# Kernel optimization log

Hardware: AMD Instinct MI355X
Metric: run time of the kernel (lower is better)

The kernel has to match this reference:

```python
import jax, jax.numpy as jnp
import numpy as np

NUM_HEADS = 16
THETA = 10000.0

def _rope(t, token_ids, theta):
    # t: [B, H, S, Dk]; token_ids: [S]
    d_k = t.shape[-1]
    inv_freq = theta ** (-jnp.arange(0, d_k, 2, dtype=jnp.float32) / d_k)  # [Dk/2]
    ang = token_ids.astype(jnp.float32)[:, None] * inv_freq[None, :]       # [S, Dk/2]
    cos, sin = jnp.cos(ang), jnp.sin(ang)
    x1, x2 = t[..., ::2], t[..., 1::2]
    r1 = x1 * cos - x2 * sin
    r2 = x1 * sin + x2 * cos
    return jnp.stack([r1, r2], axis=-1).reshape(t.shape)

def setup_inputs() -> dict:
    key = jax.random.key(0)
    ks = jax.random.split(key, 5)
    d_model = 1024
    scale = 0.02
    return {
        "x": jax.random.normal(ks[0], (4, 2048, d_model), dtype=jnp.float32),
        "token_ids": jnp.arange(2048, dtype=jnp.int32),
        "Wq": jax.random.normal(ks[1], (d_model, d_model), dtype=jnp.float32) * scale,
        "Wk": jax.random.normal(ks[2], (d_model, d_model), dtype=jnp.float32) * scale,
        "Wv": jax.random.normal(ks[3], (d_model, d_model), dtype=jnp.float32) * scale,
        "Wo": jax.random.normal(ks[4], (d_model, d_model), dtype=jnp.float32) * scale,
    }

def reference(x, token_ids, Wq, Wk, Wv, Wo):
    B, S, D = x.shape
    H = NUM_HEADS
    Dk = D // H
    def split_heads(t):
        return t.reshape(B, S, H, Dk).transpose(0, 2, 1, 3)  # [B,H,S,Dk]
    q = split_heads(x @ Wq.T)
    k = split_heads(x @ Wk.T)
    v = split_heads(x @ Wv.T)
    q = _rope(q, token_ids, THETA)
    k = _rope(k, token_ids, THETA)
    scores = jnp.einsum("bhqd,bhkd->bhqk", q, k) / jnp.sqrt(jnp.float32(Dk))
    causal = jnp.tril(jnp.ones((S, S), dtype=bool))
    scores = jnp.where(causal, scores, jnp.float32(-1e9))
    attn = jax.nn.softmax(scores, axis=-1)
    out = jnp.einsum("bhqk,bhkd->bhqd", attn, v)
    out = out.transpose(0, 2, 1, 3).reshape(B, S, H * Dk)
    return out @ Wo.T
```

## Files before the change

kernel.cpp:

```cpp
#include <hip/hip_runtime.h>

#define BATCH 4
#define SLEN 2048
#define DMODEL 1024
#define NHEADS 16
#define DK 64
#define MROWS (BATCH * SLEN)
#define NQB 16
#define SCALE_LOG2E 0.1803368801111731f

typedef short bf16x8 __attribute__((ext_vector_type(8)));
typedef unsigned short u16x4 __attribute__((ext_vector_type(4)));
typedef float f32x4 __attribute__((ext_vector_type(4)));

__device__ __forceinline__ unsigned short f2bf(float f) {
    unsigned u = __float_as_uint(f);
    unsigned r = u + 0x7FFFu + ((u >> 16) & 1u);
    return (unsigned short)(r >> 16);
}

__device__ __forceinline__ unsigned pkbf(float a, float b) {
    unsigned r;
    asm volatile("v_cvt_pk_bf16_f32 %0, %1, %2" : "=v"(r) : "v"(a), "v"(b));
    return r;
}

__device__ __forceinline__ void gload_lds16(const void* g, void* l) {
    __builtin_amdgcn_global_load_lds(
        (const __attribute__((address_space(1))) void*)g,
        (__attribute__((address_space(3))) void*)l, 16, 0, 0);
}

__global__ void cvt_f32_bf16(const float* __restrict__ in, unsigned short* __restrict__ out, int n) {
    int i = (blockIdx.x * blockDim.x + threadIdx.x) * 4;
    if (i >= n) return;
    float4 v = *reinterpret_cast<const float4*>(in + i);
    u16x4 o;
    o[0] = f2bf(v.x); o[1] = f2bf(v.y); o[2] = f2bf(v.z); o[3] = f2bf(v.w);
    *reinterpret_cast<u16x4*>(out + i) = o;
}

__global__ void cvt_w_all(const float* __restrict__ w0, const float* __restrict__ w1,
                          const float* __restrict__ w2, const float* __restrict__ w3,
                          unsigned short* __restrict__ o0, unsigned short* __restrict__ o1,
                          unsigned short* __restrict__ o2, unsigned short* __restrict__ o3) {
    int z = blockIdx.y;
    const float* src = (z == 0) ? w0 : (z == 1) ? w1 : (z == 2) ? w2 : w3;
    unsigned short* dst = (z == 0) ? o0 : (z == 1) ? o1 : (z == 2) ? o2 : o3;
    int i = (blockIdx.x * blockDim.x + threadIdx.x) * 4;
    float4 v = *reinterpret_cast<const float4*>(src + i);
    u16x4 o;
    o[0] = f2bf(v.x); o[1] = f2bf(v.y); o[2] = f2bf(v.z); o[3] = f2bf(v.w);
    *reinterpret_cast<u16x4*>(dst + i) = o;
}

__global__ void rope_table(const int* __restrict__ tok, float* __restrict__ cs, float* __restrict__ sn) {
    int idx = blockIdx.x * blockDim.x + threadIdx.x;
    if (idx >= SLEN * 32) return;
    int s = idx >> 5, fi = idx & 31;
    float invf = powf(10000.0f, -(float)(2 * fi) / 64.0f);
    float ang = (float)tok[s] * invf;
    cs[idx] = cosf(ang);
    sn[idx] = sinf(ang);
}

__global__ __launch_bounds__(256) void qkv_gemm(
    const unsigned short* __restrict__ X,
    const unsigned short* __restrict__ Wq,
    const unsigned short* __restrict__ Wk,
    const unsigned short* __restrict__ Wv,
    const float* __restrict__ cs_tab, const float* __restrict__ sn_tab,
    unsigned short* __restrict__ Q, unsigned short* __restrict__ K,
    unsigned short* __restrict__ VT)
{
    __shared__ alignas(16) unsigned short Bs[3][64 * 64];
    const int tid = threadIdx.x, lane = tid & 63, wave = tid >> 6;
    const int ln = lane & 15, kq = lane >> 4;
    const int wr = wave >> 1, wc = wave & 1;
    const int m0 = blockIdx.x * 128;
    const int n0 = blockIdx.y * 64;
    const unsigned short* Ws[3] = {Wq, Wk, Wv};

    f32x4 acc[3][4][2];
#pragma unroll
    for (int z = 0; z < 3; z++)
#pragma unroll
        for (int a = 0; a < 4; a++)
#pragma unroll
            for (int b = 0; b < 2; b++) acc[z][a][b] = (f32x4){0.f, 0.f, 0.f, 0.f};

    const unsigned short* Abase = X + (size_t)(m0 + wr * 64 + ln) * DMODEL + kq * 8;

    for (int k0 = 0; k0 < DMODEL; k0 += 64) {
        if (k0) __syncthreads();
#pragma unroll
        for (int z = 0; z < 3; z++)
#pragma unroll
            for (int i = 0; i < 2; i++) {
                int s = i * 256 + tid;
                int r = s >> 3;
                int u = (s & 7) ^ (r & 7);
                gload_lds16(Ws[z] + (size_t)(n0 + r) * DMODEL + k0 + u * 8,
                            &Bs[z][(i * 256 + wave * 64) * 8]);
            }
        __syncthreads();

        bf16x8 af[4][2];
#pragma unroll
        for (int mt = 0; mt < 4; mt++)
#pragma unroll
            for (int kc = 0; kc < 2; kc++)
                af[mt][kc] = *reinterpret_cast<const bf16x8*>(
                    Abase + (size_t)mt * 16 * DMODEL + k0 + kc * 32);

#pragma unroll
        for (int z = 0; z < 3; z++) {
            bf16x8 bfr[2][2];
#pragma unroll
            for (int nt = 0; nt < 2; nt++) {
                int row = wc * 32 + nt * 16 + ln;
#pragma unroll
                for (int kc = 0; kc < 2; kc++) {
                    int u = (kc * 4 + kq) ^ (row & 7);
                    bfr[nt][kc] = *reinterpret_cast<const bf16x8*>(&Bs[z][row * 64 + u * 8]);
                }
            }
            __builtin_amdgcn_s_setprio(1);
#pragma unroll
            for (int kc = 0; kc < 2; kc++)
#pragma unroll
                for (int mt = 0; mt < 4; mt++)
#pragma unroll
                    for (int nt = 0; nt < 2; nt++)
                        acc[z][mt][nt] = __builtin_amdgcn_mfma_f32_16x16x32_bf16(
                            af[mt][kc], bfr[nt][kc], acc[z][mt][nt], 0, 0, 0);
            __builtin_amdgcn_s_setprio(0);
        }
    }

    int m0w = m0 + wr * 64;
    int n0w = n0 + wc * 32;
#pragma unroll
    for (int z = 0; z < 2; z++) {
        unsigned short* dst = z ? K : Q;
#pragma unroll
        for (int nt = 0; nt < 2; nt++) {
            int n = n0w + nt * 16 + ln;
            int h = n >> 6, d = n & 63;
            int fi = d >> 1;
#pragma unroll
            for (int mt = 0; mt < 4; mt++) {
#pragma unroll
                for (int j = 0; j < 4; j++) {
                    int m = m0w + mt * 16 + kq * 4 + j;
                    int b = m >> 11, s = m & (SLEN - 1);
                    float v = acc[z][mt][nt][j];
                    float c = cs_tab[s * 32 + fi];
                    float si = sn_tab[s * 32 + fi];
                    float p = __shfl_xor(v, 1);
                    v = (d & 1) ? (p * si + v * c) : (v * c - p * si);
                    if (z == 0) v *= SCALE_LOG2E;
                    dst[(((size_t)(b * NHEADS + h) * SLEN + s) << 6) + d] = f2bf(v);
                }
            }
        }
    }
#pragma unroll
    for (int nt = 0; nt < 2; nt++) {
        int n = n0w + nt * 16 + ln;
        int h = n >> 6, d = n & 63;
#pragma unroll
        for (int mt = 0; mt < 4; mt++) {
#pragma unroll
            for (int j = 0; j < 4; j++) {
                int m = m0w + mt * 16 + kq * 4 + j;
                int b = m >> 11, s = m & (SLEN - 1);
                VT[((size_t)(b * NHEADS + h) * DK + d) * SLEN + s] = f2bf(acc[2][mt][nt][j]);
            }
        }
    }
}

__device__ __forceinline__ void gemm128_core_sb(
    const unsigned short* __restrict__ A, const unsigned short* __restrict__ B,
    int m0, int n0, int tid, f32x4 (&acc)[4][4],
    unsigned short* As, unsigned short* Bs)
{
    int lane = tid & 63, wave = tid >> 6;
    int ln = lane & 15, kq = lane >> 4;
    int wr = wave >> 1, wc = wave & 1;
#pragma unroll
    for (int a = 0; a < 4; a++)
#pragma unroll
        for (int b = 0; b < 4; b++) acc[a][b] = (f32x4){0.f, 0.f, 0.f, 0.f};

    for (int k0 = 0; k0 < DMODEL; k0 += 64) {
        if (k0) __syncthreads();
#pragma unroll
        for (int i = 0; i < 4; i++) {
            int s = i * 256 + tid;
            int r = s >> 3;
            int u = (s & 7) ^ (r & 7);
            gload_lds16(A + (size_t)(m0 + r) * DMODEL + k0 + u * 8, &As[(i * 256 + wave * 64) * 8]);
            gload_lds16(B + (size_t)(n0 + r) * DMODEL + k0 + u * 8, &Bs[(i * 256 + wave * 64) * 8]);
        }
        __syncthreads();

        bf16x8 af[4][2], bfr[4][2];
#pragma unroll
        for (int mt = 0; mt < 4; mt++) {
            int row = wr * 64 + mt * 16 + ln;
#pragma unroll
            for (int kc = 0; kc < 2; kc++) {
                int u = (kc * 4 + kq) ^ (row & 7);
                af[mt][kc] = *reinterpret_cast<const bf16x8*>(&As[row * 64 + u * 8]);
            }
        }
#pragma unroll
        for (int nt = 0; nt < 4; nt++) {
            int row = wc * 64 + nt * 16 + ln;
#pragma unroll
            for (int kc = 0; kc < 2; kc++) {
                int u = (kc * 4 + kq) ^ (row & 7);
                bfr[nt][kc] = *reinterpret_cast<const bf16x8*>(&Bs[row * 64 + u * 8]);
            }
        }
        __builtin_amdgcn_s_setprio(1);
#pragma unroll
        for (int kc = 0; kc < 2; kc++)
#pragma unroll
            for (int mt = 0; mt < 4; mt++)
#pragma unroll
                for (int nt = 0; nt < 4; nt++)
                    acc[mt][nt] = __builtin_amdgcn_mfma_f32_16x16x32_bf16(af[mt][kc], bfr[nt][kc], acc[mt][nt], 0, 0, 0);
        __builtin_amdgcn_s_setprio(0);
    }
}

__global__ __launch_bounds__(512, 4) void attn_kernel(
    const unsigned short* __restrict__ Q, const unsigned short* __restrict__ K,
    const unsigned short* __restrict__ VT, unsigned short* __restrict__ O)
{
    __shared__ alignas(16) unsigned short Kt[2][4096];
    __shared__ alignas(16) unsigned short Vt[2][4096];

    int tid = threadIdx.x, lane = tid & 63, wave = tid >> 6;
    int ln = lane & 15, kq = lane >> 4;
    int qb = blockIdx.x;
    int h = blockIdx.y, b = blockIdx.z;
    size_t headoff = ((size_t)b * NHEADS + h) * SLEN * DK;
    const unsigned short* Qh = Q + headoff;
    const unsigned short* Kh = K + headoff;
    const unsigned short* Vh = VT + headoff;

    auto stage = [&](int buf, int t) {
        int kv0 = t << 6;
        int s = tid;
        int r = s >> 3;
        int cb = (s & 7) ^ (r & 7);
        int rp = ((r >> 5) << 5) | (((r >> 2) & 3) << 3) | (((r >> 4) & 1) << 2) | (r & 3);
        gload_lds16(Kh + (size_t)(kv0 + rp) * DK + cb * 8, &Kt[buf][(wave * 64) * 8]);
        gload_lds16(Vh + (size_t)r * SLEN + kv0 + cb * 8, &Vt[buf][(wave * 64) * 8]);
    };

    const int q0A = (NQB - 1 - qb) * 128 + wave * 16;
    const int q0B = qb * 128 + wave * 16;
    const int ntA = 2 * (NQB - 1 - qb) + 2;
    const int tmaxA = (q0A + 15) >> 6;
    const int tmaxB = (q0B + 15) >> 6;

    bf16x8 aqA[2], aqB[2];
#pragma unroll
    for (int kc = 0; kc < 2; kc++) {
        aqA[kc] = *reinterpret_cast<const bf16x8*>(Qh + (size_t)(q0A + ln) * DK + kc * 32 + kq * 8);
        aqB[kc] = *reinterpret_cast<const bf16x8*>(Qh + (size_t)(q0B + ln) * DK + kc * 32 + kq * 8);
    }

    f32x4 oaccA[4], oaccB[4];
#pragma unroll
    for (int nt = 0; nt < 4; nt++) {
        oaccA[nt] = (f32x4){0.f, 0.f, 0.f, 0.f};
        oaccB[nt] = (f32x4){0.f, 0.f, 0.f, 0.f};
    }
    float mA = -1e30f, lA = 0.f, mB = -1e30f, lB = 0.f;

    stage(0, 0);
    __syncthreads();

    for (int t = 0; t < ntA; t++) {
        int buf = t & 1;
        if (t + 1 < ntA) stage(buf ^ 1, t + 1);
        int kv0 = t << 6;

        auto strip = [&](int q0, bf16x8 (&aq)[2], f32x4 (&oacc)[4], float& m_r, float& l_r) {
            f32x4 sacc[4];
#pragma unroll
            for (int nt = 0; nt < 4; nt++) sacc[nt] = (f32x4){0.f, 0.f, 0.f, 0.f};
            __builtin_amdgcn_s_setprio(1);
#pragma unroll
            for (int nt = 0; nt < 4; nt++) {
                int rr = nt * 16 + ln;
#pragma unroll
                for (int kc = 0; kc < 2; kc++) {
                    int unit = (kc * 4 + kq) ^ (rr & 7);
                    bf16x8 bk = *reinterpret_cast<const bf16x8*>(&Kt[buf][rr * 64 + unit * 8]);
                    sacc[nt] = __builtin_amdgcn_mfma_f32_16x16x32_bf16(bk, aq[kc], sacc[nt], 0, 0, 0);
                }
            }
            __builtin_amdgcn_s_setprio(0);

            if (kv0 + 63 > q0) {
                int q = q0 + ln;
#pragma unroll
                for (int nt = 0; nt < 4; nt++)
#pragma unroll
                    for (int j = 0; j < 4; j++) {
                        int k = kv0 + (nt >> 1) * 32 + kq * 8 + (nt & 1) * 4 + j;
                        if (k > q) sacc[nt][j] = -1e30f;
                    }
            }

            f32x4 m4 = sacc[0];
#pragma unroll
            for (int nt = 1; nt < 4; nt++) {
                m4[0] = fmaxf(m4[0], sacc[nt][0]);
                m4[1] = fmaxf(m4[1], sacc[nt][1]);
                m4[2] = fmaxf(m4[2], sacc[nt][2]);
                m4[3] = fmaxf(m4[3], sacc[nt][3]);
            }
            float mloc = fmaxf(fmaxf(m4[0], m4[1]), fmaxf(m4[2], m4[3]));
            mloc = fmaxf(mloc, __shfl_xor(mloc, 16));
            mloc = fmaxf(mloc, __shfl_xor(mloc, 32));

            bool needscale = !__all(mloc <= m_r + 8.0f);
            float so = 1.f;
            if (needscale) {
                float mn = fmaxf(m_r, mloc);
                so = exp2f(m_r - mn);
                m_r = mn;
            }

            float rs = 0.f;
#pragma unroll
            for (int nt = 0; nt < 4; nt++)
#pragma unroll
                for (int j = 0; j < 4; j++) {
                    float p = exp2f(sacc[nt][j] - m_r);
                    sacc[nt][j] = p;
                    rs += p;
                }
            rs += __shfl_xor(rs, 16);
            rs += __shfl_xor(rs, 32);
            l_r = l_r * so + rs;

            if (needscale) {
                float so_o[4];
#pragma unroll
                for (int j = 0; j < 4; j++) so_o[j] = __shfl(so, kq * 4 + j, 16);
#pragma unroll
                for (int nt = 0; nt < 4; nt++)
#pragma unroll
                    for (int j = 0; j < 4; j++)
                        oacc[nt][j] *= so_o[j];
            }

            bf16x8 pa[2];
#pragma unroll
            for (int kc = 0; kc < 2; kc++) {
                union { unsigned u[4]; bf16x8 v; } r;
                r.u[0] = pkbf(sacc[2 * kc][0], sacc[2 * kc][1]);
                r.u[1] = pkbf(sacc[2 * kc][2], sacc[2 * kc][3]);
                r.u[2] = pkbf(sacc[2 * kc + 1][0], sacc[2 * kc + 1][1]);
                r.u[3] = pkbf(sacc[2 * kc + 1][2], sacc[2 * kc + 1][3]);
                pa[kc] = r.v;
            }

            __builtin_amdgcn_s_setprio(1);
#pragma unroll
            for (int nt = 0; nt < 4; nt++) {
                int rr = nt * 16 + ln;
#pragma unroll
                for (int kc = 0; kc < 2; kc++) {
                    int unit = (kc * 4 + kq) ^ (rr & 7);
                    bf16x8 bv = *reinterpret_cast<const bf16x8*>(&Vt[buf][rr * 64 + unit * 8]);
                    oacc[nt] = __builtin_amdgcn_mfma_f32_16x16x32_bf16(pa[kc], bv, oacc[nt], 0, 0, 0);
                }
            }
            __builtin_amdgcn_s_setprio(0);
        };

        if (t <= tmaxA) strip(q0A, aqA, oaccA, mA, lA);
        if (t <= tmaxB) strip(q0B, aqB, oaccB, mB, lB);

        __syncthreads();
    }

    {
        float lo[4];
#pragma unroll
        for (int j = 0; j < 4; j++) lo[j] = __shfl(lA, kq * 4 + j, 16);
#pragma unroll
        for (int nt = 0; nt < 4; nt++)
#pragma unroll
            for (int j = 0; j < 4; j++) {
                int row = q0A + kq * 4 + j;
                O[((size_t)b * SLEN + row) * DMODEL + h * 64 + nt * 16 + ln] = f2bf(oaccA[nt][j] / lo[j]);
            }
    }
    {
        float lo[4];
#pragma unroll
        for (int j = 0; j < 4; j++) lo[j] = __shfl(lB, kq * 4 + j, 16);
#pragma unroll
        for (int nt = 0; nt < 4; nt++)
#pragma unroll
            for (int j = 0; j < 4; j++) {
                int row = q0B + kq * 4 + j;
                O[((size_t)b * SLEN + row) * DMODEL + h * 64 + nt * 16 + ln] = f2bf(oaccB[nt][j] / lo[j]);
            }
    }
}

__global__ __launch_bounds__(256) void out_gemm(
    const unsigned short* __restrict__ A, const unsigned short* __restrict__ Wo,
    float* __restrict__ out)
{
    __shared__ alignas(16) unsigned short As[128 * 64];
    __shared__ alignas(16) unsigned short Bs[128 * 64];
    int tid = threadIdx.x, lane = tid & 63, wave = tid >> 6;
    int ln = lane & 15, kq = lane >> 4;
    int wr = wave >> 1, wc = wave & 1;
    int m0 = blockIdx.x * 128;
    int n0 = blockIdx.y * 128;

    f32x4 acc[4][4];
    gemm128_core_sb(A, Wo, m0, n0, tid, acc, As, Bs);

    int m0w = m0 + wr * 64, n0w = n0 + wc * 64;
#pragma unroll
    for (int mt = 0; mt < 4; mt++)
#pragma unroll
        for (int nt = 0; nt < 4; nt++)
#pragma unroll
            for (int j = 0; j < 4; j++) {
                int m = m0w + mt * 16 + kq * 4 + j;
                int n = n0w + nt * 16 + ln;
                out[(size_t)m * DMODEL + n] = acc[mt][nt][j];
            }
}

extern "C" void kernel_launch(void* const* d_in, const int* in_sizes, int n_in,
                              void* d_out, int out_size, void* d_ws, size_t ws_size,
                              hipStream_t stream) {
    const float* x  = (const float*)d_in[0];
    const int* tok  = (const int*)d_in[1];
    const float* wq = (const float*)d_in[2];
    const float* wk = (const float*)d_in[3];
    const float* wv = (const float*)d_in[4];
    const float* wo = (const float*)d_in[5];
    float* out = (float*)d_out;

    const size_t XB_OFF = 0;
    const size_t WQ_OFF = 16777216;
    const size_t WK_OFF = 18874368;
    const size_t WV_OFF = 20971520;
    const size_t WO_OFF = 23068672;
    const size_t Q_OFF  = 25165824;
    const size_t K_OFF  = 41943040;
    const size_t VT_OFF = 58720256;
    const size_t O_OFF  = 75497472;
    const size_t CS_OFF = 92274688;
    const size_t SN_OFF = 92536832;
    const size_t WS_NEEDED = 92798976;
    if (ws_size < WS_NEEDED) return;

    char* ws = (char*)d_ws;
    unsigned short* Xb  = (unsigned short*)(ws + XB_OFF);
    unsigned short* Wqb = (unsigned short*)(ws + WQ_OFF);
    unsigned short* Wkb = (unsigned short*)(ws + WK_OFF);
    unsigned short* Wvb = (unsigned short*)(ws + WV_OFF);
    unsigned short* Wob = (unsigned short*)(ws + WO_OFF);
    unsigned short* Qb  = (unsigned short*)(ws + Q_OFF);
    unsigned short* Kb  = (unsigned short*)(ws + K_OFF);
    unsigned short* VTb = (unsigned short*)(ws + VT_OFF);
    unsigned short* Ob  = (unsigned short*)(ws + O_OFF);
    float* cs_tab = (float*)(ws + CS_OFF);
    float* sn_tab = (float*)(ws + SN_OFF);

    cvt_f32_bf16<<<8192, 256, 0, stream>>>(x, Xb, MROWS * DMODEL);
    cvt_w_all<<<dim3(1024, 4), 256, 0, stream>>>(wq, wk, wv, wo, Wqb, Wkb, Wvb, Wob);
    rope_table<<<256, 256, 0, stream>>>(tok, cs_tab, sn_tab);

    qkv_gemm<<<dim3(MROWS / 128, DMODEL / 64, 1), 256, 0, stream>>>(
        Xb, Wqb, Wkb, Wvb, cs_tab, sn_tab, Qb, Kb, VTb);

    attn_kernel<<<dim3(SLEN / 256, NHEADS, BATCH), 512, 0, stream>>>(Qb, Kb, VTb, Ob);

    out_gemm<<<dim3(MROWS / 128, DMODEL / 128, 1), 256, 0, stream>>>(Ob, Wob, out);
}
```

Before: 260.2 us.

## Restructure QKV GEMM into 256x256 LDS-tiled, double-buffered pipelined kernel

The QKV projection now uses 512-thread blocks that each compute a 256x256 output tile for a single weight matrix, selected by blockIdx.y. Previously each block computed 128x64 tiles for all three weights and read X straight from global memory. Both X and W tiles are now staged in swizzled LDS using async global-to-LDS loads, split into halves and double-buffered across k-steps with explicit vmcnt waits and barriers. This raises operand reuse per byte loaded and overlaps loads with MFMA work. In exchange it uses about 128KB of LDS per block, adds more barriers, and launches only 384 blocks, which may leave the last wave underfilled.

```diff
diff --git a/kernel.cpp b/kernel.cpp
--- a/kernel.cpp
+++ b/kernel.cpp
@@ -64,7 +64,7 @@
     sn[idx] = sinf(ang);
 }
 
-__global__ __launch_bounds__(256) void qkv_gemm(
+__global__ __launch_bounds__(512, 2) void qkv_gemm(
     const unsigned short* __restrict__ X,
     const unsigned short* __restrict__ Wq,
     const unsigned short* __restrict__ Wk,
@@ -73,110 +73,137 @@
     unsigned short* __restrict__ Q, unsigned short* __restrict__ K,
     unsigned short* __restrict__ VT)
 {
-    __shared__ alignas(16) unsigned short Bs[3][64 * 64];
+    __shared__ alignas(16) unsigned short Al[2][2][128 * 64];
+    __shared__ alignas(16) unsigned short Bl[2][2][128 * 64];
     const int tid = threadIdx.x, lane = tid & 63, wave = tid >> 6;
     const int ln = lane & 15, kq = lane >> 4;
-    const int wr = wave >> 1, wc = wave & 1;
-    const int m0 = blockIdx.x * 128;
-    const int n0 = blockIdx.y * 64;
-    const unsigned short* Ws[3] = {Wq, Wk, Wv};
-
-    f32x4 acc[3][4][2];
-#pragma unroll
-    for (int z = 0; z < 3; z++)
-#pragma unroll
-        for (int a = 0; a < 4; a++)
-#pragma unroll
-            for (int b = 0; b < 2; b++) acc[z][a][b] = (f32x4){0.f, 0.f, 0.f, 0.f};
-
-    const unsigned short* Abase = X + (size_t)(m0 + wr * 64 + ln) * DMODEL + kq * 8;
-
-    for (int k0 = 0; k0 < DMODEL; k0 += 64) {
-        if (k0) __syncthreads();
-#pragma unroll
-        for (int z = 0; z < 3; z++)
-#pragma unroll
-            for (int i = 0; i < 2; i++) {
-                int s = i * 256 + tid;
-                int r = s >> 3;
-                int u = (s & 7) ^ (r & 7);
-                gload_lds16(Ws[z] + (size_t)(n0 + r) * DMODEL + k0 + u * 8,
-                            &Bs[z][(i * 256 + wave * 64) * 8]);
-            }
-        __syncthreads();
-
-        bf16x8 af[4][2];
-#pragma unroll
-        for (int mt = 0; mt < 4; mt++)
+    const int wm = wave >> 2, wn = wave & 3;
+    const int m0 = blockIdx.x * 256;
+    const int z = blockIdx.y >> 2;
+    const int n0 = (blockIdx.y & 3) * 256;
+    const unsigned short* W = (z == 0) ? Wq : (z == 1) ? Wk : Wv;
+
+    auto stA = [&](int buf, int mh, int kt) {
+#pragma unroll
+        for (int l = 0; l < 2; l++) {
+            int s = l * 512 + tid;
+            int pr = s >> 3;
+            int u = (s & 7) ^ (pr & 7);
+            int grow = m0 + ((pr >> 6) << 7) + mh * 64 + (pr & 63);
+            gload_lds16(X + (size_t)grow * DMODEL + kt * 64 + u * 8,
+                        &Al[buf][mh][(l * 512 + wave * 64) * 8]);
+        }
+    };
+    auto stB = [&](int buf, int nh, int kt) {
+#pragma unroll
+        for (int l = 0; l < 2; l++) {
+            int s = l * 512 + tid;
+            int pc = s >> 3;
+            int u = (s & 7) ^ (pc & 7);
+            int gcol = n0 + ((pc >> 5) << 6) + nh * 32 + (pc & 31);
+            gload_lds16(W + (size_t)gcol * DMODEL + kt * 64 + u * 8,
+                        &Bl[buf][nh][(l * 512 + wave * 64) * 8]);
+        }
+    };
+
+    f32x4 acc[8][4];
+#pragma unroll
+    for (int a = 0; a < 8; a++)
+#pragma unroll
+        for (int b = 0; b < 4; b++) acc[a][b] = (f32x4){0.f, 0.f, 0.f, 0.f};
+
+    stA(0, 0, 0); stB(0, 0, 0); stA(0, 1, 0); stB(0, 1, 0);
+    stA(1, 0, 1); stB(1, 0, 1);
+    asm volatile("s_waitcnt vmcnt(0)" ::: "memory");
+    __builtin_amdgcn_s_barrier();
+
+    const int NK = DMODEL / 64;
+    for (int kt = 0; kt < NK; ++kt) {
+        const int buf = kt & 1;
+#pragma unroll
+        for (int p = 0; p < 4; ++p) {
+            const int mh = p >> 1, nh = p & 1;
+            bf16x8 af[4][2], bq[2][2];
+#pragma unroll
+            for (int i = 0; i < 4; i++) {
+                int pr = wm * 64 + i * 16 + ln;
+#pragma unroll
+                for (int kc = 0; kc < 2; kc++) {
+                    int u = (kc * 4 + kq) ^ (pr & 7);
+                    af[i][kc] = *reinterpret_cast<const bf16x8*>(&Al[buf][mh][(pr * 8 + u) * 8]);
+                }
+            }
+#pragma unroll
+            for (int f = 0; f < 2; f++) {
+                int pc = wn * 32 + f * 16 + ln;
+#pragma unroll
+                for (int kc = 0; kc < 2; kc++) {
+                    int u = (kc * 4 + kq) ^ (pc & 7);
+                    bq[f][kc] = *reinterpret_cast<const bf16x8*>(&Bl[buf][nh][(pc * 8 + u) * 8]);
+                }
+            }
+            if (p == 0 && kt + 1 < NK) stA(buf ^ 1, 1, kt + 1);
+            if (p == 1 && kt + 1 < NK) stB(buf ^ 1, 1, kt + 1);
+            if (p == 2 && kt + 2 < NK) stA(buf, 0, kt + 2);
+            if (p == 3 && kt + 2 < NK) stB(buf, 0, kt + 2);
+            if (kt == NK - 1) {
+                if (p == 0) { asm volatile("s_waitcnt vmcnt(0)" ::: "memory"); }
+            } else {
+                asm volatile("s_waitcnt vmcnt(6)" ::: "memory");
+            }
+            __builtin_amdgcn_s_barrier();
+            asm volatile("s_waitcnt lgkmcnt(0)" ::: "memory");
+            __builtin_amdgcn_sched_barrier(0);
+            __builtin_amdgcn_s_setprio(1);
 #pragma unroll
             for (int kc = 0; kc < 2; kc++)
-                af[mt][kc] = *reinterpret_cast<const bf16x8*>(
-                    Abase + (size_t)mt * 16 * DMODEL + k0 + kc * 32);
-
-#pragma unroll
-        for (int z = 0; z < 3; z++) {
-            bf16x8 bfr[2][2];
-#pragma unroll
-            for (int nt = 0; nt < 2; nt++) {
-                int row = wc * 32 + nt * 16 + ln;
-#pragma unroll
-                for (int kc = 0; kc < 2; kc++) {
-                    int u = (kc * 4 + kq) ^ (row & 7);
-                    bfr[nt][kc] = *reinterpret_cast<const bf16x8*>(&Bs[z][row * 64 + u * 8]);
-                }
-            }
-            __builtin_amdgcn_s_setprio(1);
-#pragma unroll
-            for (int kc = 0; kc < 2; kc++)
-#pragma unroll
-                for (int mt = 0; mt < 4; mt++)
-#pragma unroll
-                    for (int nt = 0; nt < 2; nt++)
-                        acc[z][mt][nt] = __builtin_amdgcn_mfma_f32_16x16x32_bf16(
-                            af[mt][kc], bfr[nt][kc], acc[z][mt][nt], 0, 0, 0);
+#pragma unroll
+                for (int i = 0; i < 4; i++)
+#pragma unroll
+                    for (int f = 0; f < 2; f++)
+                        acc[mh * 4 + i][nh * 2 + f] = __builtin_amdgcn_mfma_f32_16x16x32_bf16(
+                            af[i][kc], bq[f][kc], acc[mh * 4 + i][nh * 2 + f], 0, 0, 0);
             __builtin_amdgcn_s_setprio(0);
-        }
-    }
-
-    int m0w = m0 + wr * 64;
-    int n0w = n0 + wc * 32;
-#pragma unroll
-    for (int z = 0; z < 2; z++) {
+            __builtin_amdgcn_s_barrier();
+        }
+    }
+
+    if (z < 2) {
         unsigned short* dst = z ? K : Q;
 #pragma unroll
-        for (int nt = 0; nt < 2; nt++) {
-            int n = n0w + nt * 16 + ln;
+        for (int b = 0; b < 4; b++) {
+            int n = n0 + wn * 64 + (b >> 1) * 32 + (b & 1) * 16 + ln;
             int h = n >> 6, d = n & 63;
             int fi = d >> 1;
 #pragma unroll
-            for (int mt = 0; mt < 4; mt++) {
+            for (int a = 0; a < 8; a++) {
 #pragma unroll
                 for (int j = 0; j < 4; j++) {
-                    int m = m0w + mt * 16 + kq * 4 + j;
-                    int b = m >> 11, s = m & (SLEN - 1);
-                    float v = acc[z][mt][nt][j];
+                    int m = m0 + wm * 128 + (a >> 2) * 64 + (a & 3) * 16 + kq * 4 + j;
+                    int bb = m >> 11, s = m & (SLEN - 1);
+                    float v = acc[a][b][j];
                     float c = cs_tab[s * 32 + fi];
                     float si = sn_tab[s * 32 + fi];
-                    float p = __shfl_xor(v, 1);
-                    v = (d & 1) ? (p * si + v * c) : (v * c - p * si);
+                    float pz = __shfl_xor(v, 1);
+                    v = (d & 1) ? (pz * si + v * c) : (v * c - pz * si);
                     if (z == 0) v *= SCALE_LOG2E;
-                    dst[(((size_t)(b * NHEADS + h) * SLEN + s) << 6) + d] = f2bf(v);
-                }
-            }
-        }
-    }
-#pragma unroll
-    for (int nt = 0; nt < 2; nt++) {
-        int n = n0w + nt * 16 + ln;
-        int h = n >> 6, d = n & 63;
-#pragma unroll
-        for (int mt = 0; mt < 4; mt++) {
-#pragma unroll
-            for (int j = 0; j < 4; j++) {
-                int m = m0w + mt * 16 + kq * 4 + j;
-                int b = m >> 11, s = m & (SLEN - 1);
-                VT[((size_t)(b * NHEADS + h) * DK + d) * SLEN + s] = f2bf(acc[2][mt][nt][j]);
-            }
+                    dst[(((size_t)(bb * NHEADS + h) * SLEN + s) << 6) + d] = f2bf(v);
+                }
+            }
+        }
+    } else {
+#pragma unroll
+        for (int b = 0; b < 4; b++) {
+            int n = n0 + wn * 64 + (b >> 1) * 32 + (b & 1) * 16 + ln;
+            int h = n >> 6, d = n & 63;
+#pragma unroll
+            for (int a = 0; a < 8; a++)
+#pragma unroll
+                for (int j = 0; j < 4; j++) {
+                    int m = m0 + wm * 128 + (a >> 2) * 64 + (a & 3) * 16 + kq * 4 + j;
+                    int bb = m >> 11, s = m & (SLEN - 1);
+                    VT[((size_t)(bb * NHEADS + h) * DK + d) * SLEN + s] = f2bf(acc[a][b][j]);
+                }
         }
     }
 }
@@ -491,7 +518,7 @@
     cvt_w_all<<<dim3(1024, 4), 256, 0, stream>>>(wq, wk, wv, wo, Wqb, Wkb, Wvb, Wob);
     rope_table<<<256, 256, 0, stream>>>(tok, cs_tab, sn_tab);
 
-    qkv_gemm<<<dim3(MROWS / 128, DMODEL / 64, 1), 256, 0, stream>>>(
+    qkv_gemm<<<dim3(MROWS / 256, 12, 1), 512, 0, stream>>>(
         Xb, Wqb, Wkb, Wvb, cs_tab, sn_tab, Qb, Kb, VTb);
 
     attn_kernel<<<dim3(SLEN / 256, NHEADS, BATCH), 512, 0, stream>>>(Qb, Kb, VTb, Ob);
```

Measured after the change: 214.9 us. -17.4%, faster.
